# Performance work log

Measured on AMD Instinct MI355X. Metric: run time of the kernel, lower is better.

## Reference

```python
import jax, jax.numpy as jnp
import numpy as np


def setup_inputs() -> dict:
    key = jax.random.key(0)
    k1, k2, k3, k4, k5 = jax.random.split(key, 5)
    B, S, D = 16, 1024, 64
    query = jax.random.normal(k1, (B, S, D), dtype=jnp.float32)
    key_t = jax.random.normal(k2, (B, S, D), dtype=jnp.float32)
    value = jax.random.normal(k3, (B, S, D), dtype=jnp.float32)
    t_m = jax.random.uniform(k4, (B, S, S), dtype=jnp.float32)
    g_m = jax.random.uniform(k5, (B, S, S), dtype=jnp.float32)
    # causal mask [S, S]: 1 where attention allowed
    mask = jnp.tril(jnp.ones((S, S), dtype=jnp.int32))
    return {"query": query, "key": key_t, "value": value,
            "t_m": t_m, "g_m": g_m, "mask": mask}


def _bias(m):
    # per-batch max over all S*S entries, then abs difference
    mx = jnp.max(m.reshape(m.shape[0], -1), axis=1)  # [B]
    return jnp.abs(m - mx[:, None, None])            # [B, S, S]


def reference(query, key, value, t_m, g_m, mask):
    d_k = query.shape[-1]
    # NOTE: source divides by d_k, not sqrt(d_k)
    scores = jnp.einsum('bqd,bkd->bqk', query, key) / d_k  # [B, S, S]
    scores = scores + _bias(t_m) + _bias(g_m)
    scores = jnp.where(mask[None, :, :] == 0, jnp.float32(-1e9), scores)
    p_attn = jax.nn.softmax(scores, axis=-1)
    return jnp.einsum('bqk,bkd->bqd', p_attn, value)
```

## Files before the change

kernel.cpp:

```cpp
#include <hip/hip_runtime.h>
#include <hip/hip_bf16.h>

#define B_  16
#define S_  1024
#define D_  64

typedef __attribute__((ext_vector_type(8))) short bf16x8;
typedef __attribute__((ext_vector_type(4))) float f32x4;

__device__ __forceinline__ unsigned short f2bf_u(float f) {
    __hip_bfloat16 h = __float2bfloat16(f);
    return __builtin_bit_cast(unsigned short, h);
}
__device__ __forceinline__ short f2bf(float f) {
    return (short)f2bf_u(f);
}
__device__ __forceinline__ unsigned pk2(float a, float b) {
    return (unsigned)f2bf_u(a) | ((unsigned)f2bf_u(b) << 16);
}

__global__ __launch_bounds__(256) void prep_kernel(
    const float* __restrict__ K, const float* __restrict__ V,
    unsigned short* __restrict__ Kbf, unsigned short* __restrict__ VT)
{
    const int bid = blockIdx.x;
    if (bid < 512) {
        const size_t i = ((size_t)bid * 256 + threadIdx.x) * 8;
        const float4 x = *(const float4*)(K + i);
        const float4 y = *(const float4*)(K + i + 4);
        uint4 o = { pk2(x.x, x.y), pk2(x.z, x.w), pk2(y.x, y.y), pk2(y.z, y.w) };
        *(uint4*)(Kbf + i) = o;
    } else {
        const int i  = (bid - 512) * 256 + threadIdx.x;
        const int d  = i & 63;
        const int kg = (i >> 6) & 127;
        const int b  = i >> 13;
        const float* vp = V + ((size_t)b * S_ + (size_t)kg * 8) * D_ + d;
        const float v0 = vp[0],   v1 = vp[64],  v2 = vp[128], v3 = vp[192];
        const float v4 = vp[256], v5 = vp[320], v6 = vp[384], v7 = vp[448];
        uint4 o = { pk2(v0, v1), pk2(v2, v3), pk2(v4, v5), pk2(v6, v7) };
        *(uint4*)(VT + ((size_t)b * D_ + d) * S_ + kg * 8) = o;
    }
}

__global__ __launch_bounds__(256, 4) void attn_mfma_pre(
    const unsigned short* __restrict__ Kbf, const unsigned short* __restrict__ VT,
    const float* __restrict__ Q, const float* __restrict__ t_m,
    const float* __restrict__ g_m, float* __restrict__ out)
{
    __shared__ __align__(16) char smem[17920];
    unsigned short (*s_p)[136] = (unsigned short (*)[136])smem;
    float* cmb = (float*)smem;
    float* cml = (float*)(smem + 17408);

    const int bid = blockIdx.x;
    const int b   = bid & 15;
    const int g   = bid >> 4;
    const int qt  = (g < 32) ? (63 - g) : (g - 32);
    const int qb  = qt << 4;
    const int tid = threadIdx.x;
    const int w   = tid >> 6;
    const int ln  = tid & 63;
    const int lg  = ln >> 4;
    const int lm  = ln & 15;

    const size_t biasb = (size_t)b * S_ * S_;
    const float* tmb = t_m + biasb + (size_t)(qb + 4 * lg) * S_ + lm;
    const float* gmb = g_m + biasb + (size_t)(qb + 4 * lg) * S_ + lm;

    const unsigned short* Kbb = Kbf + ((size_t)(b * S_) + lm) * D_ + 8 * lg;
    const unsigned short* vt0 = VT + ((size_t)(b * D_) + 0  + lm) * S_ + 8 * lg;
    const unsigned short* vt1 = VT + ((size_t)(b * D_) + 16 + lm) * S_ + 8 * lg;
    const unsigned short* vt2 = VT + ((size_t)(b * D_) + 32 + lm) * S_ + 8 * lg;
    const unsigned short* vt3 = VT + ((size_t)(b * D_) + 48 + lm) * S_ + 8 * lg;

    bf16x8 qa[2];
    #pragma unroll
    for (int ks = 0; ks < 2; ++ks) {
        const float* qp = Q + ((size_t)(b * S_) + qb + lm) * D_ + 32 * ks + 8 * lg;
        const float4 x = *(const float4*)qp;
        const float4 y = *(const float4*)(qp + 4);
        bf16x8 f;
        f[0] = f2bf(x.x); f[1] = f2bf(x.y);
        f[2] = f2bf(x.z); f[3] = f2bf(x.w);
        f[4] = f2bf(y.x); f[5] = f2bf(y.y);
        f[6] = f2bf(y.z); f[7] = f2bf(y.w);
        qa[ks] = f;
    }

    float mrun[4] = {-1e30f, -1e30f, -1e30f, -1e30f};
    float lrun[4] = {0.f, 0.f, 0.f, 0.f};
    const f32x4 z4 = {0.f, 0.f, 0.f, 0.f};
    f32x4 oacc[4] = {z4, z4, z4, z4};

    const int ntw = ((qb + 15 - 32 * w) >> 7) + 1;

    for (int t = 0; t < ntw; ++t) {
        const int ke = (t << 7) + 32 * w;

        const bf16x8* kp = (const bf16x8*)(Kbb + (size_t)ke * D_);
        bf16x8 kf00 = kp[0];
        bf16x8 kf01 = *(const bf16x8*)((const unsigned short*)kp + 32);
        bf16x8 kf10 = *(const bf16x8*)((const unsigned short*)kp + 16 * D_);
        bf16x8 kf11 = *(const bf16x8*)((const unsigned short*)kp + 16 * D_ + 32);

        const bf16x8 vb0 = *(const bf16x8*)(vt0 + ke);
        const bf16x8 vb1 = *(const bf16x8*)(vt1 + ke);
        const bf16x8 vb2 = *(const bf16x8*)(vt2 + ke);
        const bf16x8 vb3 = *(const bf16x8*)(vt3 + ke);

        float bt[2][4], bg[2][4];
        #pragma unroll
        for (int nf = 0; nf < 2; ++nf)
            #pragma unroll
            for (int r = 0; r < 4; ++r) {
                const size_t off = (size_t)r * S_ + ke + 16 * nf;
                bt[nf][r] = tmb[off];
                bg[nf][r] = gmb[off];
            }

        f32x4 sa[2] = {z4, z4};
        sa[0] = __builtin_amdgcn_mfma_f32_16x16x32_bf16(qa[0], kf00, sa[0], 0, 0, 0);
        sa[0] = __builtin_amdgcn_mfma_f32_16x16x32_bf16(qa[1], kf01, sa[0], 0, 0, 0);
        sa[1] = __builtin_amdgcn_mfma_f32_16x16x32_bf16(qa[0], kf10, sa[1], 0, 0, 0);
        sa[1] = __builtin_amdgcn_mfma_f32_16x16x32_bf16(qa[1], kf11, sa[1], 0, 0, 0);

        float p[2][4], tmax[4];
        #pragma unroll
        for (int r = 0; r < 4; ++r) {
            const int qg = qb + 4 * lg + r;
            float s0 = sa[0][r] * (1.f / 64.f) - bt[0][r] - bg[0][r];
            float s1 = sa[1][r] * (1.f / 64.f) - bt[1][r] - bg[1][r];
            if (ke + lm > qg)      s0 = -1e30f;
            if (ke + 16 + lm > qg) s1 = -1e30f;
            p[0][r] = s0;  p[1][r] = s1;
            tmax[r] = fmaxf(s0, s1);
        }
        #pragma unroll
        for (int off = 1; off < 16; off <<= 1)
            #pragma unroll
            for (int r = 0; r < 4; ++r)
                tmax[r] = fmaxf(tmax[r], __shfl_xor(tmax[r], off, 64));

        #pragma unroll
        for (int r = 0; r < 4; ++r) {
            const float mn = fmaxf(mrun[r], tmax[r]);
            const float a  = __expf(mrun[r] - mn);
            mrun[r] = mn;
            const float p0 = __expf(p[0][r] - mn);
            const float p1 = __expf(p[1][r] - mn);
            p[0][r] = p0;  p[1][r] = p1;
            float rs = p0 + p1;
            #pragma unroll
            for (int off = 1; off < 16; off <<= 1)
                rs += __shfl_xor(rs, off, 64);
            lrun[r] = lrun[r] * a + rs;
            #pragma unroll
            for (int nd = 0; nd < 4; ++nd) oacc[nd][r] *= a;
        }

        #pragma unroll
        for (int nf = 0; nf < 2; ++nf)
            #pragma unroll
            for (int r = 0; r < 4; ++r)
                s_p[4 * lg + r][32 * w + 16 * nf + lm] = f2bf_u(p[nf][r]);
        asm volatile("s_waitcnt lgkmcnt(0)" ::: "memory");
        const bf16x8 pa = *(const bf16x8*)&s_p[lm][32 * w + 8 * lg];

        oacc[0] = __builtin_amdgcn_mfma_f32_16x16x32_bf16(pa, vb0, oacc[0], 0, 0, 0);
        oacc[1] = __builtin_amdgcn_mfma_f32_16x16x32_bf16(pa, vb1, oacc[1], 0, 0, 0);
        oacc[2] = __builtin_amdgcn_mfma_f32_16x16x32_bf16(pa, vb2, oacc[2], 0, 0, 0);
        oacc[3] = __builtin_amdgcn_mfma_f32_16x16x32_bf16(pa, vb3, oacc[3], 0, 0, 0);
    }

    __syncthreads();
    #pragma unroll
    for (int nd = 0; nd < 4; ++nd)
        #pragma unroll
        for (int r = 0; r < 4; ++r)
            cmb[(w * 16 + 4 * lg + r) * 68 + 16 * nd + lm] = oacc[nd][r];
    if (lm == 0) {
        #pragma unroll
        for (int r = 0; r < 4; ++r) {
            cml[w * 32 + 4 * lg + r]      = mrun[r];
            cml[w * 32 + 16 + 4 * lg + r] = lrun[r];
        }
    }
    __syncthreads();
    {
        const int q = tid >> 4, c = tid & 15;
        float mm[4], sc[4];
        float ms = -1e30f;
        #pragma unroll
        for (int i = 0; i < 4; ++i) { mm[i] = cml[i * 32 + q]; ms = fmaxf(ms, mm[i]); }
        float lt = 0.f;
        #pragma unroll
        for (int i = 0; i < 4; ++i) {
            sc[i] = __expf(mm[i] - ms);
            lt += cml[i * 32 + 16 + q] * sc[i];
        }
        const float inv = 1.f / lt;
        float4 acc = make_float4(0.f, 0.f, 0.f, 0.f);
        #pragma unroll
        for (int i = 0; i < 4; ++i) {
            const float4 v = *(const float4*)&cmb[(i * 16 + q) * 68 + 4 * c];
            acc.x += v.x * sc[i];  acc.y += v.y * sc[i];
            acc.z += v.z * sc[i];  acc.w += v.w * sc[i];
        }
        acc.x *= inv; acc.y *= inv; acc.z *= inv; acc.w *= inv;
        *(float4*)(out + ((size_t)(b * S_) + qb + q) * D_ + 4 * c) = acc;
    }
}

__global__ __launch_bounds__(256, 4) void attn_mfma_kernel(
    const float* __restrict__ Q, const float* __restrict__ K,
    const float* __restrict__ V, const float* __restrict__ t_m,
    const float* __restrict__ g_m, float* __restrict__ out)
{
    __shared__ __align__(16) char smem[17920];
    unsigned short (*s_p)[136] = (unsigned short (*)[136])smem;
    float* cmb = (float*)smem;
    float* cml = (float*)(smem + 17408);

    const int bid = blockIdx.x;
    const int b   = bid & 15;
    const int g   = bid >> 4;
    const int qt  = (g < 32) ? (63 - g) : (g - 32);
    const int qb  = qt << 4;
    const int tid = threadIdx.x;
    const int w   = tid >> 6;
    const int ln  = tid & 63;
    const int lg  = ln >> 4;
    const int lm  = ln & 15;

    const size_t kvb   = (size_t)(b * S_) * D_;
    const size_t biasb = (size_t)b * S_ * S_;
    const float* Kb = K + kvb;
    const float* Vb = V + kvb;

    bf16x8 qa[2];
    #pragma unroll
    for (int ks = 0; ks < 2; ++ks) {
        const float* qp = Q + ((size_t)(b * S_) + qb + lm) * D_ + 32 * ks + 8 * lg;
        const float4 x = *(const float4*)qp;
        const float4 y = *(const float4*)(qp + 4);
        bf16x8 f;
        f[0] = f2bf(x.x); f[1] = f2bf(x.y);
        f[2] = f2bf(x.z); f[3] = f2bf(x.w);
        f[4] = f2bf(y.x); f[5] = f2bf(y.y);
        f[6] = f2bf(y.z); f[7] = f2bf(y.w);
        qa[ks] = f;
    }

    float mrun[4] = {-1e30f, -1e30f, -1e30f, -1e30f};
    float lrun[4] = {0.f, 0.f, 0.f, 0.f};
    const f32x4 z4 = {0.f, 0.f, 0.f, 0.f};
    f32x4 oacc[4] = {z4, z4, z4, z4};

    const int ntw = ((qb + 15 - 32 * w) >> 7) + 1;

    for (int t = 0; t < ntw; ++t) {
        const int ke = (t << 7) + 32 * w;

        bf16x8 kf[2][2];
        #pragma unroll
        for (int nf = 0; nf < 2; ++nf)
            #pragma unroll
            for (int ks = 0; ks < 2; ++ks) {
                const float* kp = Kb + (size_t)(ke + 16 * nf + lm) * D_ + 32 * ks + 8 * lg;
                const float4 x = *(const float4*)kp;
                const float4 y = *(const float4*)(kp + 4);
                bf16x8 f;
                f[0] = f2bf(x.x); f[1] = f2bf(x.y);
                f[2] = f2bf(x.z); f[3] = f2bf(x.w);
                f[4] = f2bf(y.x); f[5] = f2bf(y.y);
                f[6] = f2bf(y.z); f[7] = f2bf(y.w);
                kf[nf][ks] = f;
            }

        float bt[2][4], bg[2][4];
        #pragma unroll
        for (int nf = 0; nf < 2; ++nf)
            #pragma unroll
            for (int r = 0; r < 4; ++r) {
                const size_t off = biasb + (size_t)(qb + 4 * lg + r) * S_
                                 + ke + 16 * nf + lm;
                bt[nf][r] = t_m[off];
                bg[nf][r] = g_m[off];
            }

        f32x4 sa[2] = {z4, z4};
        #pragma unroll
        for (int nf = 0; nf < 2; ++nf)
            #pragma unroll
            for (int ks = 0; ks < 2; ++ks)
                sa[nf] = __builtin_amdgcn_mfma_f32_16x16x32_bf16(
                    qa[ks], kf[nf][ks], sa[nf], 0, 0, 0);

        float vf[4][8];
        #pragma unroll
        for (int nd = 0; nd < 4; ++nd)
            #pragma unroll
            for (int j = 0; j < 8; ++j)
                vf[nd][j] = Vb[(size_t)(ke + 8 * lg + j) * D_ + 16 * nd + lm];

        float p[2][4], tmax[4];
        #pragma unroll
        for (int r = 0; r < 4; ++r) {
            const int qg = qb + 4 * lg + r;
            float s0 = sa[0][r] * (1.f / 64.f) - bt[0][r] - bg[0][r];
            float s1 = sa[1][r] * (1.f / 64.f) - bt[1][r] - bg[1][r];
            if (ke + lm > qg)      s0 = -1e30f;
            if (ke + 16 + lm > qg) s1 = -1e30f;
            p[0][r] = s0;  p[1][r] = s1;
            tmax[r] = fmaxf(s0, s1);
        }
        #pragma unroll
        for (int off = 1; off < 16; off <<= 1)
            #pragma unroll
            for (int r = 0; r < 4; ++r)
                tmax[r] = fmaxf(tmax[r], __shfl_xor(tmax[r], off, 64));

        #pragma unroll
        for (int r = 0; r < 4; ++r) {
            const float mn = fmaxf(mrun[r], tmax[r]);
            const float a  = __expf(mrun[r] - mn);
            mrun[r] = mn;
            const float p0 = __expf(p[0][r] - mn);
            const float p1 = __expf(p[1][r] - mn);
            p[0][r] = p0;  p[1][r] = p1;
            float rs = p0 + p1;
            #pragma unroll
            for (int off = 1; off < 16; off <<= 1)
                rs += __shfl_xor(rs, off, 64);
            lrun[r] = lrun[r] * a + rs;
            #pragma unroll
            for (int nd = 0; nd < 4; ++nd) oacc[nd][r] *= a;
        }

        #pragma unroll
        for (int nf = 0; nf < 2; ++nf)
            #pragma unroll
            for (int r = 0; r < 4; ++r)
                s_p[4 * lg + r][32 * w + 16 * nf + lm] = f2bf_u(p[nf][r]);
        asm volatile("s_waitcnt lgkmcnt(0)" ::: "memory");
        const bf16x8 pa = *(const bf16x8*)&s_p[lm][32 * w + 8 * lg];

        #pragma unroll
        for (int nd = 0; nd < 4; ++nd) {
            bf16x8 vb;
            #pragma unroll
            for (int j = 0; j < 8; ++j) vb[j] = f2bf(vf[nd][j]);
            oacc[nd] = __builtin_amdgcn_mfma_f32_16x16x32_bf16(
                pa, vb, oacc[nd], 0, 0, 0);
        }
    }

    __syncthreads();
    #pragma unroll
    for (int nd = 0; nd < 4; ++nd)
        #pragma unroll
        for (int r = 0; r < 4; ++r)
            cmb[(w * 16 + 4 * lg + r) * 68 + 16 * nd + lm] = oacc[nd][r];
    if (lm == 0) {
        #pragma unroll
        for (int r = 0; r < 4; ++r) {
            cml[w * 32 + 4 * lg + r]      = mrun[r];
            cml[w * 32 + 16 + 4 * lg + r] = lrun[r];
        }
    }
    __syncthreads();
    {
        const int q = tid >> 4, c = tid & 15;
        float mm[4], sc[4];
        float ms = -1e30f;
        #pragma unroll
        for (int i = 0; i < 4; ++i) { mm[i] = cml[i * 32 + q]; ms = fmaxf(ms, mm[i]); }
        float lt = 0.f;
        #pragma unroll
        for (int i = 0; i < 4; ++i) {
            sc[i] = __expf(mm[i] - ms);
            lt += cml[i * 32 + 16 + q] * sc[i];
        }
        const float inv = 1.f / lt;
        float4 acc = make_float4(0.f, 0.f, 0.f, 0.f);
        #pragma unroll
        for (int i = 0; i < 4; ++i) {
            const float4 v = *(const float4*)&cmb[(i * 16 + q) * 68 + 4 * c];
            acc.x += v.x * sc[i];  acc.y += v.y * sc[i];
            acc.z += v.z * sc[i];  acc.w += v.w * sc[i];
        }
        acc.x *= inv; acc.y *= inv; acc.z *= inv; acc.w *= inv;
        *(float4*)(out + ((size_t)(b * S_) + qb + q) * D_ + 4 * c) = acc;
    }
}

extern "C" void kernel_launch(void* const* d_in, const int* in_sizes, int n_in,
                              void* d_out, int out_size, void* d_ws, size_t ws_size,
                              hipStream_t stream) {
    const float* Q   = (const float*)d_in[0];
    const float* Kp  = (const float*)d_in[1];
    const float* V   = (const float*)d_in[2];
    const float* t_m = (const float*)d_in[3];
    const float* g_m = (const float*)d_in[4];

    const size_t need = (size_t)2 * B_ * S_ * D_ * sizeof(unsigned short);
    if (ws_size >= need) {
        unsigned short* Kbf = (unsigned short*)d_ws;
        unsigned short* VT  = Kbf + (size_t)B_ * S_ * D_;
        prep_kernel<<<1024, 256, 0, stream>>>(Kp, V, Kbf, VT);
        attn_mfma_pre<<<1024, 256, 0, stream>>>(Kbf, VT, Q, t_m, g_m,
                                                (float*)d_out);
    } else {
        attn_mfma_kernel<<<1024, 256, 0, stream>>>(Q, Kp, V, t_m, g_m,
                                                   (float*)d_out);
    }
}
```

Before: 34.24 us.

## Swap QK MFMA operands so each lane owns one query row

Swaps the A and B operands of the QK^T MFMA so the score fragment is transposed. Each lane now holds one query row and four consecutive keys per fragment. This lets the t_m and g_m bias tiles be read with float4 loads instead of scalar strided loads. It also turns the row max and sum reductions into two cross-lane shuffles on a single running max and sum per lane, and lets the probabilities be written to shared memory as packed 64-bit stores. In exchange, the rescale factor has to be broadcast back to the output accumulator layout with extra shuffles.

```diff
diff --git a/kernel.cpp b/kernel.cpp
--- a/kernel.cpp
+++ b/kernel.cpp
@@ -43,7 +43,7 @@
     }
 }
 
-__global__ __launch_bounds__(256, 4) void attn_mfma_pre(
+__global__ __launch_bounds__(256, 4) void attn_mfma_swp(
     const unsigned short* __restrict__ Kbf, const unsigned short* __restrict__ VT,
     const float* __restrict__ Q, const float* __restrict__ t_m,
     const float* __restrict__ g_m, float* __restrict__ out)
@@ -65,8 +65,8 @@
     const int lm  = ln & 15;
 
     const size_t biasb = (size_t)b * S_ * S_;
-    const float* tmb = t_m + biasb + (size_t)(qb + 4 * lg) * S_ + lm;
-    const float* gmb = g_m + biasb + (size_t)(qb + 4 * lg) * S_ + lm;
+    const float* tmb = t_m + biasb + (size_t)(qb + lm) * S_ + 4 * lg;
+    const float* gmb = g_m + biasb + (size_t)(qb + lm) * S_ + 4 * lg;
 
     const unsigned short* Kbb = Kbf + ((size_t)(b * S_) + lm) * D_ + 8 * lg;
     const unsigned short* vt0 = VT + ((size_t)(b * D_) + 0  + lm) * S_ + 8 * lg;
@@ -88,8 +88,8 @@
         qa[ks] = f;
     }
 
-    float mrun[4] = {-1e30f, -1e30f, -1e30f, -1e30f};
-    float lrun[4] = {0.f, 0.f, 0.f, 0.f};
+    float mrun = -1e30f;
+    float lrun = 0.f;
     const f32x4 z4 = {0.f, 0.f, 0.f, 0.f};
     f32x4 oacc[4] = {z4, z4, z4, z4};
 
@@ -98,72 +98,78 @@
     for (int t = 0; t < ntw; ++t) {
         const int ke = (t << 7) + 32 * w;
 
-        const bf16x8* kp = (const bf16x8*)(Kbb + (size_t)ke * D_);
-        bf16x8 kf00 = kp[0];
-        bf16x8 kf01 = *(const bf16x8*)((const unsigned short*)kp + 32);
-        bf16x8 kf10 = *(const bf16x8*)((const unsigned short*)kp + 16 * D_);
-        bf16x8 kf11 = *(const bf16x8*)((const unsigned short*)kp + 16 * D_ + 32);
+        const float4 bt0 = *(const float4*)(tmb + ke);
+        const float4 bt1 = *(const float4*)(tmb + ke + 16);
+        const float4 bg0 = *(const float4*)(gmb + ke);
+        const float4 bg1 = *(const float4*)(gmb + ke + 16);
+
+        const unsigned short* kp = Kbb + (size_t)ke * D_;
+        const bf16x8 kf00 = *(const bf16x8*)kp;
+        const bf16x8 kf01 = *(const bf16x8*)(kp + 32);
+        const bf16x8 kf10 = *(const bf16x8*)(kp + 16 * D_);
+        const bf16x8 kf11 = *(const bf16x8*)(kp + 16 * D_ + 32);
 
         const bf16x8 vb0 = *(const bf16x8*)(vt0 + ke);
         const bf16x8 vb1 = *(const bf16x8*)(vt1 + ke);
         const bf16x8 vb2 = *(const bf16x8*)(vt2 + ke);
         const bf16x8 vb3 = *(const bf16x8*)(vt3 + ke);
 
-        float bt[2][4], bg[2][4];
-        #pragma unroll
-        for (int nf = 0; nf < 2; ++nf)
+        f32x4 sa0 = z4, sa1 = z4;
+        sa0 = __builtin_amdgcn_mfma_f32_16x16x32_bf16(kf00, qa[0], sa0, 0, 0, 0);
+        sa0 = __builtin_amdgcn_mfma_f32_16x16x32_bf16(kf01, qa[1], sa0, 0, 0, 0);
+        sa1 = __builtin_amdgcn_mfma_f32_16x16x32_bf16(kf10, qa[0], sa1, 0, 0, 0);
+        sa1 = __builtin_amdgcn_mfma_f32_16x16x32_bf16(kf11, qa[1], sa1, 0, 0, 0);
+
+        const int qg = qb + lm;
+        const int k0 = ke + 4 * lg;
+        float s[8];
+        {
+            const float b0[4] = {bt0.x + bg0.x, bt0.y + bg0.y,
+                                 bt0.z + bg0.z, bt0.w + bg0.w};
+            const float b1[4] = {bt1.x + bg1.x, bt1.y + bg1.y,
+                                 bt1.z + bg1.z, bt1.w + bg1.w};
             #pragma unroll
             for (int r = 0; r < 4; ++r) {
-                const size_t off = (size_t)r * S_ + ke + 16 * nf;
-                bt[nf][r] = tmb[off];
-                bg[nf][r] = gmb[off];
+                float v0 = sa0[r] * (1.f / 64.f) - b0[r];
+                float v1 = sa1[r] * (1.f / 64.f) - b1[r];
+                if (k0 + r > qg)      v0 = -1e30f;
+                if (k0 + 16 + r > qg) v1 = -1e30f;
+                s[r]     = v0;
+                s[4 + r] = v1;
             }
-
-        f32x4 sa[2] = {z4, z4};
-        sa[0] = __builtin_amdgcn_mfma_f32_16x16x32_bf16(qa[0], kf00, sa[0], 0, 0, 0);
-        sa[0] = __builtin_amdgcn_mfma_f32_16x16x32_bf16(qa[1], kf01, sa[0], 0, 0, 0);
-        sa[1] = __builtin_amdgcn_mfma_f32_16x16x32_bf16(qa[0], kf10, sa[1], 0, 0, 0);
-        sa[1] = __builtin_amdgcn_mfma_f32_16x16x32_bf16(qa[1], kf11, sa[1], 0, 0, 0);
-
-        float p[2][4], tmax[4];
-        #pragma unroll
-        for (int r = 0; r < 4; ++r) {
-            const int qg = qb + 4 * lg + r;
-            float s0 = sa[0][r] * (1.f / 64.f) - bt[0][r] - bg[0][r];
-            float s1 = sa[1][r] * (1.f / 64.f) - bt[1][r] - bg[1][r];
-            if (ke + lm > qg)      s0 = -1e30f;
-            if (ke + 16 + lm > qg) s1 = -1e30f;
-            p[0][r] = s0;  p[1][r] = s1;
-            tmax[r] = fmaxf(s0, s1);
-        }
-        #pragma unroll
-        for (int off = 1; off < 16; off <<= 1)
+        }
+
+        float tmax = fmaxf(fmaxf(fmaxf(s[0], s[1]), fmaxf(s[2], s[3])),
+                           fmaxf(fmaxf(s[4], s[5]), fmaxf(s[6], s[7])));
+        tmax = fmaxf(tmax, __shfl_xor(tmax, 16, 64));
+        tmax = fmaxf(tmax, __shfl_xor(tmax, 32, 64));
+        const float mn = fmaxf(mrun, tmax);
+        const float a  = __expf(mrun - mn);
+        mrun = mn;
+        float p[8];
+        float rs = 0.f;
+        #pragma unroll
+        for (int i = 0; i < 8; ++i) { p[i] = __expf(s[i] - mn); rs += p[i]; }
+        rs += __shfl_xor(rs, 16, 64);
+        rs += __shfl_xor(rs, 32, 64);
+        lrun = lrun * a + rs;
+
+        float ar[4];
+        #pragma unroll
+        for (int r = 0; r < 4; ++r) ar[r] = __shfl(a, 4 * lg + r, 64);
+        #pragma unroll
+        for (int nd = 0; nd < 4; ++nd)
             #pragma unroll
             for (int r = 0; r < 4; ++r)
-                tmax[r] = fmaxf(tmax[r], __shfl_xor(tmax[r], off, 64));
-
-        #pragma unroll
-        for (int r = 0; r < 4; ++r) {
-            const float mn = fmaxf(mrun[r], tmax[r]);
-            const float a  = __expf(mrun[r] - mn);
-            mrun[r] = mn;
-            const float p0 = __expf(p[0][r] - mn);
-            const float p1 = __expf(p[1][r] - mn);
-            p[0][r] = p0;  p[1][r] = p1;
-            float rs = p0 + p1;
-            #pragma unroll
-            for (int off = 1; off < 16; off <<= 1)
-                rs += __shfl_xor(rs, off, 64);
-            lrun[r] = lrun[r] * a + rs;
-            #pragma unroll
-            for (int nd = 0; nd < 4; ++nd) oacc[nd][r] *= a;
-        }
-
-        #pragma unroll
-        for (int nf = 0; nf < 2; ++nf)
-            #pragma unroll
-            for (int r = 0; r < 4; ++r)
-                s_p[4 * lg + r][32 * w + 16 * nf + lm] = f2bf_u(p[nf][r]);
+                oacc[nd][r] *= ar[r];
+
+        {
+            unsigned u0 = pk2(p[0], p[1]), u1 = pk2(p[2], p[3]);
+            unsigned u2 = pk2(p[4], p[5]), u3 = pk2(p[6], p[7]);
+            unsigned short* row = &s_p[lm][32 * w + 4 * lg];
+            *(uint2*)row        = make_uint2(u0, u1);
+            *(uint2*)(row + 16) = make_uint2(u2, u3);
+        }
         asm volatile("s_waitcnt lgkmcnt(0)" ::: "memory");
         const bf16x8 pa = *(const bf16x8*)&s_p[lm][32 * w + 8 * lg];
 
@@ -179,12 +185,9 @@
         #pragma unroll
         for (int r = 0; r < 4; ++r)
             cmb[(w * 16 + 4 * lg + r) * 68 + 16 * nd + lm] = oacc[nd][r];
-    if (lm == 0) {
-        #pragma unroll
-        for (int r = 0; r < 4; ++r) {
-            cml[w * 32 + 4 * lg + r]      = mrun[r];
-            cml[w * 32 + 16 + 4 * lg + r] = lrun[r];
-        }
+    if (ln < 16) {
+        cml[w * 32 + ln]      = mrun;
+        cml[w * 32 + 16 + ln] = lrun;
     }
     __syncthreads();
     {
@@ -409,7 +412,7 @@
         unsigned short* Kbf = (unsigned short*)d_ws;
         unsigned short* VT  = Kbf + (size_t)B_ * S_ * D_;
         prep_kernel<<<1024, 256, 0, stream>>>(Kp, V, Kbf, VT);
-        attn_mfma_pre<<<1024, 256, 0, stream>>>(Kbf, VT, Q, t_m, g_m,
+        attn_mfma_swp<<<1024, 256, 0, stream>>>(Kbf, VT, Q, t_m, g_m,
                                                 (float*)d_out);
     } else {
         attn_mfma_kernel<<<1024, 256, 0, stream>>>(Q, Kp, V, t_m, g_m,
```

New measurement: 36.69 us. 7.2% more time.

## Split causal attention key range across two blocks and add combine kernel

Applied to the files above, without the earlier changes.

Launches twice as many attention blocks, each processing alternating 128-key chunks, and writes unnormalized partial outputs plus per-row max and sum to workspace. A new combine kernel merges the two partials with rescaling and normalizes. This aims to raise parallelism and shorten the longest blocks in the causal workload. The cost is an extra kernel launch and round-trip traffic for the partial results.

```diff
diff --git a/kernel.cpp b/kernel.cpp
--- a/kernel.cpp
+++ b/kernel.cpp
@@ -43,10 +43,11 @@
     }
 }
 
-__global__ __launch_bounds__(256, 4) void attn_mfma_pre(
+__global__ __launch_bounds__(256, 4) void attn_mfma_split(
     const unsigned short* __restrict__ Kbf, const unsigned short* __restrict__ VT,
     const float* __restrict__ Q, const float* __restrict__ t_m,
-    const float* __restrict__ g_m, float* __restrict__ out)
+    const float* __restrict__ g_m, float* __restrict__ opart,
+    float* __restrict__ mlpart)
 {
     __shared__ __align__(16) char smem[17920];
     unsigned short (*s_p)[136] = (unsigned short (*)[136])smem;
@@ -54,8 +55,10 @@
     float* cml = (float*)(smem + 17408);
 
     const int bid = blockIdx.x;
-    const int b   = bid & 15;
-    const int g   = bid >> 4;
+    const int h   = bid >> 10;
+    const int low = bid & 1023;
+    const int b   = low & 15;
+    const int g   = low >> 4;
     const int qt  = (g < 32) ? (63 - g) : (g - 32);
     const int qb  = qt << 4;
     const int tid = threadIdx.x;
@@ -93,16 +96,17 @@
     const f32x4 z4 = {0.f, 0.f, 0.f, 0.f};
     f32x4 oacc[4] = {z4, z4, z4, z4};
 
-    const int ntw = ((qb + 15 - 32 * w) >> 7) + 1;
+    const int base_w = 128 * h + 32 * w;
+    const int ntw = ((qb + 15 - base_w) >> 8) + 1;
 
     for (int t = 0; t < ntw; ++t) {
-        const int ke = (t << 7) + 32 * w;
-
-        const bf16x8* kp = (const bf16x8*)(Kbb + (size_t)ke * D_);
-        bf16x8 kf00 = kp[0];
-        bf16x8 kf01 = *(const bf16x8*)((const unsigned short*)kp + 32);
-        bf16x8 kf10 = *(const bf16x8*)((const unsigned short*)kp + 16 * D_);
-        bf16x8 kf11 = *(const bf16x8*)((const unsigned short*)kp + 16 * D_ + 32);
+        const int ke = (t << 8) + base_w;
+
+        const unsigned short* kp = Kbb + (size_t)ke * D_;
+        const bf16x8 kf00 = *(const bf16x8*)kp;
+        const bf16x8 kf01 = *(const bf16x8*)(kp + 32);
+        const bf16x8 kf10 = *(const bf16x8*)(kp + 16 * D_);
+        const bf16x8 kf11 = *(const bf16x8*)(kp + 16 * D_ + 32);
 
         const bf16x8 vb0 = *(const bf16x8*)(vt0 + ke);
         const bf16x8 vb1 = *(const bf16x8*)(vt1 + ke);
@@ -199,7 +203,6 @@
             sc[i] = __expf(mm[i] - ms);
             lt += cml[i * 32 + 16 + q] * sc[i];
         }
-        const float inv = 1.f / lt;
         float4 acc = make_float4(0.f, 0.f, 0.f, 0.f);
         #pragma unroll
         for (int i = 0; i < 4; ++i) {
@@ -207,9 +210,41 @@
             acc.x += v.x * sc[i];  acc.y += v.y * sc[i];
             acc.z += v.z * sc[i];  acc.w += v.w * sc[i];
         }
-        acc.x *= inv; acc.y *= inv; acc.z *= inv; acc.w *= inv;
-        *(float4*)(out + ((size_t)(b * S_) + qb + q) * D_ + 4 * c) = acc;
-    }
+        *(float4*)(opart + ((size_t)bid * 16 + q) * D_ + 4 * c) = acc;
+        if (c == 0) {
+            mlpart[bid * 32 + q]      = ms;
+            mlpart[bid * 32 + 16 + q] = lt;
+        }
+    }
+}
+
+__global__ __launch_bounds__(256) void combine_kernel(
+    const float* __restrict__ opart, const float* __restrict__ mlpart,
+    float* __restrict__ out)
+{
+    const int bid = blockIdx.x;
+    const int b   = bid & 15;
+    const int g   = bid >> 4;
+    const int qt  = (g < 32) ? (63 - g) : (g - 32);
+    const int qb  = qt << 4;
+    const int q   = threadIdx.x >> 4, c = threadIdx.x & 15;
+    const int p0  = bid, p1 = bid + 1024;
+
+    const float m0 = mlpart[p0 * 32 + q], l0 = mlpart[p0 * 32 + 16 + q];
+    const float m1 = mlpart[p1 * 32 + q], l1 = mlpart[p1 * 32 + 16 + q];
+    const float M  = fmaxf(m0, m1);
+    const float s0 = __expf(m0 - M);
+    const float s1 = __expf(m1 - M);
+    const float inv = 1.f / (l0 * s0 + l1 * s1);
+
+    const float4 a0 = *(const float4*)(opart + ((size_t)p0 * 16 + q) * D_ + 4 * c);
+    const float4 a1 = *(const float4*)(opart + ((size_t)p1 * 16 + q) * D_ + 4 * c);
+    float4 o;
+    o.x = (a0.x * s0 + a1.x * s1) * inv;
+    o.y = (a0.y * s0 + a1.y * s1) * inv;
+    o.z = (a0.z * s0 + a1.z * s1) * inv;
+    o.w = (a0.w * s0 + a1.w * s1) * inv;
+    *(float4*)(out + ((size_t)(b * S_) + qb + q) * D_ + 4 * c) = o;
 }
 
 __global__ __launch_bounds__(256, 4) void attn_mfma_kernel(
@@ -404,13 +439,20 @@
     const float* t_m = (const float*)d_in[3];
     const float* g_m = (const float*)d_in[4];
 
-    const size_t need = (size_t)2 * B_ * S_ * D_ * sizeof(unsigned short);
+    const size_t n_kv    = (size_t)B_ * S_ * D_;
+    const size_t opart_f = (size_t)2048 * 16 * D_;
+    const size_t mlpart_f = (size_t)2048 * 32;
+    const size_t need = 2 * n_kv * sizeof(unsigned short)
+                      + (opart_f + mlpart_f) * sizeof(float);
     if (ws_size >= need) {
         unsigned short* Kbf = (unsigned short*)d_ws;
-        unsigned short* VT  = Kbf + (size_t)B_ * S_ * D_;
+        unsigned short* VT  = Kbf + n_kv;
+        float* opart  = (float*)(VT + n_kv);
+        float* mlpart = opart + opart_f;
         prep_kernel<<<1024, 256, 0, stream>>>(Kp, V, Kbf, VT);
-        attn_mfma_pre<<<1024, 256, 0, stream>>>(Kbf, VT, Q, t_m, g_m,
-                                                (float*)d_out);
+        attn_mfma_split<<<2048, 256, 0, stream>>>(Kbf, VT, Q, t_m, g_m,
+                                                  opart, mlpart);
+        combine_kernel<<<1024, 256, 0, stream>>>(opart, mlpart, (float*)d_out);
     } else {
         attn_mfma_kernel<<<1024, 256, 0, stream>>>(Q, Kp, V, t_m, g_m,
                                                    (float*)d_out);
```

Measured after the change: 40.70 us. +18.9%, slower.
